# Performance work log

Hardware: AMD Instinct MI355X
Metric: run time of the kernel (lower is better)

## Reference

```python
import jax, jax.numpy as jnp
import numpy as np
from jax import lax

B = 512
P_KEEP = 0.5  # base dropout keep probability (p=0.5)


def conv(x, w, b, pad):
    y = lax.conv_general_dilated(x, w, (1, 1), [(pad, pad), (pad, pad)],
                                 dimension_numbers=('NCHW', 'OIHW', 'NCHW'))
    return y + b[None, :, None, None]


def maxpool3s2(x):
    return lax.reduce_window(x, -jnp.inf, lax.max, (1, 1, 3, 3), (1, 1, 2, 2), 'VALID')


def eb_linear(p_out, a, W):
    # Excitation backprop through a linear layer (bias ignored).
    # p_out: [B, out] marginal winning probs at layer output
    # a:     [B, in]  (non-negative) activations at layer input
    # W:     [out, in]
    Wp = jnp.maximum(W, 0.0)
    z = a @ Wp.T                              # [B, out]
    s = jnp.where(z > 0, p_out / z, 0.0)      # [B, out]
    return a * (s @ Wp)                       # [B, in]


def setup_inputs() -> dict:
    key = jax.random.key(0)
    ks = jax.random.split(key, 16)

    def w(k, shape, fan_in):
        return (jax.random.normal(k, shape, jnp.float32) / np.sqrt(fan_in)).astype(jnp.float32)

    return {
        'x': jax.random.normal(ks[0], (B, 3, 32, 32), jnp.float32),
        'noise': jax.random.uniform(ks[1], (B, 2048), jnp.float32),
        'conv1_w': w(ks[2], (96, 3, 5, 5), 3 * 25),
        'conv1_b': jnp.zeros((96,), jnp.float32),
        'conv2_w': w(ks[3], (128, 96, 5, 5), 96 * 25),
        'conv2_b': jnp.zeros((128,), jnp.float32),
        'conv3_w': w(ks[4], (256, 128, 5, 5), 128 * 25),
        'conv3_b': jnp.zeros((256,), jnp.float32),
        'fc1_w': w(ks[5], (2048, 1024), 1024),
        'fc1_b': jnp.zeros((2048,), jnp.float32),
        'fc2_w': w(ks[6], (2048, 2048), 2048),
        'fc2_b': jnp.zeros((2048,), jnp.float32),
        'fc3_w': w(ks[7], (10, 2048), 2048),
        'fc3_b': jnp.zeros((10,), jnp.float32),
        'label': jax.random.randint(ks[8], (B,), 0, 10),
    }


def reference(x, noise, conv1_w, conv1_b, conv2_w, conv2_b, conv3_w, conv3_b,
              fc1_w, fc1_b, fc2_w, fc2_b, fc3_w, fc3_b, label):
    h1 = maxpool3s2(jax.nn.relu(conv(x, conv1_w, conv1_b, 1)))   # [B,96,14,14]
    h2 = maxpool3s2(jax.nn.relu(conv(h1, conv2_w, conv2_b, 2)))  # [B,128,6,6]
    h3 = maxpool3s2(jax.nn.relu(conv(h2, conv3_w, conv3_b, 2)))  # [B,256,2,2]
    h4 = h3.reshape(h3.shape[0], -1)                             # [B,1024]
    h5 = jax.nn.relu(h4 @ fc1_w.T + fc1_b)                       # [B,2048]

    # --- Excitation backprop through latterModel (fc2 -> relu -> fc3), batched ---
    h6_eb = jax.nn.relu(h5 @ fc2_w.T + fc2_b)                    # [B,2048]
    p_out = jax.nn.one_hot(label, 10, dtype=h5.dtype)            # [B,10]
    p_h6 = eb_linear(p_out, h6_eb, fc3_w)                        # [B,2048]
    pebs = eb_linear(p_h6, h5, fc2_w)                            # [B,2048]

    # --- Excitation Dropout mask ---
    N = pebs.shape[1]
    num = (1.0 - P_KEEP) * (N - 1) * pebs
    retain_p = 1.0 - num / (num + P_KEEP * (1.0 - pebs))         # [B,2048]
    mask = (noise < retain_p).astype(h5.dtype)
    h_ed = jnp.where(retain_p > 0, h5 * mask / retain_p, 0.0)

    h6 = jax.nn.relu(h_ed @ fc2_w.T + fc2_b)                     # [B,2048]
    return h6 @ fc3_w.T + fc3_b                                  # [B,10]
```

## Files before the change

kernel.cpp:

```cpp
#include <hip/hip_runtime.h>
#include <hip/hip_bf16.h>


typedef __attribute__((ext_vector_type(8))) short bf16x8;
typedef __attribute__((ext_vector_type(4))) float f32x4;

__device__ __forceinline__ void split_bf16(float x, ushort& h, ushort& l) {
    __hip_bfloat16 bh = __float2bfloat16(x);
    float fh = __bfloat162float(bh);
    __hip_bfloat16 bl = __float2bfloat16(x - fh);
    h = *(ushort*)&bh;
    l = *(ushort*)&bl;
}

__device__ __forceinline__ void split3_bf16(float x, ushort& a, ushort& b,
                                            ushort& c) {
    __hip_bfloat16 ba = __float2bfloat16(x);
    float fa = __bfloat162float(ba);
    float r = x - fa;
    __hip_bfloat16 bb = __float2bfloat16(r);
    float fb = __bfloat162float(bb);
    __hip_bfloat16 bc = __float2bfloat16(r - fb);
    a = *(ushort*)&ba;
    b = *(ushort*)&bb;
    c = *(ushort*)&bc;
}

__device__ __forceinline__ void gld_lds16(const void* g, void* l) {
    __builtin_amdgcn_global_load_lds(
        (const __attribute__((address_space(1))) unsigned int*)g,
        (__attribute__((address_space(3))) unsigned int*)l, 16, 0, 0);
}

__global__ void zero_k(float4* __restrict__ p, int n4) {
    int idx = blockIdx.x * 256 + threadIdx.x;
    int stride = gridDim.x * 256;
    float4 z = {0.f, 0.f, 0.f, 0.f};
    for (int i = idx; i < n4; i += stride) p[i] = z;
}

__global__ void transw_k(const float* __restrict__ in, float* __restrict__ out,
                         int OC, int K) {
    int idx = blockIdx.x * 256 + threadIdx.x;
    if (idx >= OC * K) return;
    int oc = idx / K, k = idx % K;
    out[k * OC + oc] = in[idx];
}

__global__ void splitw_k(const float* __restrict__ in, ushort* __restrict__ hi,
                         ushort* __restrict__ lo, int OC, int IC) {
    int idx = blockIdx.x * 256 + threadIdx.x;
    if (idx >= OC * IC * 25) return;
    int oc = idx / (IC * 25);
    int r = idx % (IC * 25);
    int ic = r / 25, tap = r % 25;
    float v = in[idx];
    ushort h, l;
    split_bf16(v, h, l);
    size_t k = (size_t)oc * IC * 25 + tap * IC + ic;
    hi[k] = h;
    lo[k] = l;
}

__global__ void splitw3_k(const float* __restrict__ in, ushort* __restrict__ out,
                          int off, int total) {
    int idx = blockIdx.x * 256 + threadIdx.x;
    if (idx >= total) return;
    ushort a, b, c;
    split3_bf16(in[idx], a, b, c);
    out[idx] = a;
    out[idx + off] = b;
    out[idx + 2 * off] = c;
}

__global__ __launch_bounds__(256) void splitw3t_relu_k(
        const float* __restrict__ in, ushort* __restrict__ out, int off) {
    __shared__ float tile[64][65];
    const int bx = blockIdx.x & 31, by = blockIdx.x >> 5;
    const int j = threadIdx.x & 63, i0 = threadIdx.x >> 6;
    for (int i = i0; i < 64; i += 4)
        tile[i][j] = in[(size_t)(by * 64 + i) * 2048 + bx * 64 + j];
    __syncthreads();
    for (int r = i0; r < 64; r += 4) {
        float x = fmaxf(tile[j][r], 0.f);
        ushort a, b, c;
        split3_bf16(x, a, b, c);
        size_t o = (size_t)(bx * 64 + r) * 2048 + by * 64 + j;
        out[o] = a;
        out[o + off] = b;
        out[o + 2 * off] = c;
    }
}

__global__ __launch_bounds__(256) void conv1_v3(
        const float* __restrict__ x, const float* __restrict__ w1t,
        const float* __restrict__ b1, ushort* __restrict__ h1hi,
        ushort* __restrict__ h1lo) {
    __shared__ float simg[3 * 34 * 34];
    __shared__ float c1s[8][904];
    const int b = blockIdx.x, oc0 = blockIdx.y * 8, t = threadIdx.x;

    for (int i = t; i < 3 * 34 * 34; i += 256) simg[i] = 0.f;
    __syncthreads();
    for (int i = t; i < 3072; i += 256) {
        int ic = i >> 10, r = (i >> 5) & 31, c = i & 31;
        simg[ic * 1156 + (r + 1) * 34 + (c + 1)] = x[(size_t)b * 3072 + i];
    }
    __syncthreads();

    int base[4];
    bool valid[4];
#pragma unroll
    for (int j = 0; j < 4; j++) {
        int p = t + j * 256;
        valid[j] = p < 900;
        int oh = p / 30, ow = p % 30;
        base[j] = valid[j] ? oh * 34 + ow : 0;
    }

    float acc[4][8];
#pragma unroll
    for (int j = 0; j < 4; j++)
#pragma unroll
        for (int u = 0; u < 8; u++) acc[j][u] = 0.f;

#pragma unroll 1
    for (int ic = 0; ic < 3; ic++) {
        const int icb = ic * 1156;
#pragma unroll 1
        for (int kh = 0; kh < 5; kh++) {
#pragma unroll
            for (int kw = 0; kw < 5; kw++) {
                const float4* wr =
                    (const float4*)&w1t[(ic * 25 + kh * 5 + kw) * 96 + oc0];
                float4 w0 = wr[0], w1v = wr[1];
#pragma unroll
                for (int j = 0; j < 4; j++) {
                    float v = simg[icb + base[j] + kh * 34 + kw];
#pragma unroll
                    for (int u = 0; u < 4; u++) {
                        acc[j][u] = fmaf((&w0.x)[u], v, acc[j][u]);
                        acc[j][u + 4] = fmaf((&w1v.x)[u], v, acc[j][u + 4]);
                    }
                }
            }
        }
    }
#pragma unroll
    for (int j = 0; j < 4; j++)
        if (valid[j]) {
            int p = t + j * 256;
#pragma unroll
            for (int u = 0; u < 8; u++) c1s[u][p] = acc[j][u];
        }
    __syncthreads();
    if (t < 196) {
        const int ph = t / 14, pw = t % 14;
        ushort hv[8], lv[8];
#pragma unroll
        for (int u = 0; u < 8; u++) {
            float m = c1s[u][(2 * ph) * 30 + 2 * pw];
#pragma unroll
            for (int q = 1; q < 9; q++) {
                int dy = q / 3, dx = q % 3;
                m = fmaxf(m, c1s[u][(2 * ph + dy) * 30 + 2 * pw + dx]);
            }
            float o = fmaxf(m + b1[oc0 + u], 0.f);
            split_bf16(o, hv[u], lv[u]);
        }
        size_t ob = (((size_t)b * 18 + ph + 2) * 18 + pw + 2) * 96 + oc0;
        *(bf16x8*)&h1hi[ob] = *(bf16x8*)&hv[0];
        *(bf16x8*)&h1lo[ob] = *(bf16x8*)&lv[0];
    }
}

template <int BM, int IC, int H, int W, int OH, int OW, int OC, int NM>
__global__ __launch_bounds__(256, 2) void convmfma5_k(
        const ushort* __restrict__ ah, int aoff,
        const ushort* __restrict__ wh, int boff,
        const float* __restrict__ bias, float* __restrict__ C) {
    constexpr int K = 25 * IC;
    constexpr int MI = BM / 32;
    constexpr int G = NM * (OC / 128);
    __shared__ ushort At[2][BM * 64];
    __shared__ ushort Bt[2][128 * 64];
    const int t = threadIdx.x;
    const int lane = t & 63, wv = t >> 6;
    const int id = blockIdx.x;
    const int id2 = (id & 7) * (G >> 3) + (id >> 3);
    const int n0 = (id2 / NM) * 128;
    const int m0 = (id2 % NM) * BM;
    const int wm = (wv >> 1) * (BM / 2);
    const int wn = (wv & 1) * 64;

    const int srow = lane >> 3;
    const int slot = lane & 7;
    const int part = slot ^ srow;
    const bool hiA = part < 4;
    const int pk = (part & 3) * 8;

    int arb[MI];
#pragma unroll
    for (int rr = 0; rr < MI; rr++) {
        int r = wv * (BM / 4) + rr * 8 + srow;
        int m = m0 + r;
        int b = m / (OH * OW), pxy = m % (OH * OW);
        int oh = pxy / OW, ow = pxy % OW;
        arb[rr] = ((b * H + oh) * W + ow) * IC + pk;
    }
    const ushort* __restrict__ aptr = ah + (hiA ? 0 : aoff);
    size_t brb[4];
#pragma unroll
    for (int rr = 0; rr < 4; rr++) {
        int r = wv * 32 + rr * 8 + srow;
        brb[rr] = (size_t)(n0 + r) * K + pk;
    }
    const ushort* __restrict__ bptr = wh + (hiA ? 0 : boff);

    f32x4 acc[MI][4];
#pragma unroll
    for (int i = 0; i < MI; i++)
#pragma unroll
        for (int j = 0; j < 4; j++) acc[i][j] = (f32x4)(0.f);

    const int q = lane >> 4;
    const int fr = lane & 15;

    auto stage = [&](int buf, int k0s) {
        const int tap = k0s / IC;
        const int koff = ((tap / 5) * W + (tap % 5)) * IC + (k0s - tap * IC);
#pragma unroll
        for (int rr = 0; rr < MI; rr++)
            gld_lds16(aptr + arb[rr] + koff,
                      &At[buf][(wv * (BM / 4) + rr * 8) * 64]);
#pragma unroll
        for (int rr = 0; rr < 4; rr++)
            gld_lds16(bptr + brb[rr] + k0s,
                      &Bt[buf][(wv * 32 + rr * 8) * 64]);
    };

    stage(0, 0);
    __syncthreads();

    int cur = 0;
#pragma unroll 1
    for (int k0 = 0; k0 < K; k0 += 32) {
        bf16x8 afh[MI], afl[MI], bfh[4], bfl[4];
#pragma unroll
        for (int i = 0; i < MI; i++) {
            int row = wm + fr + i * 16;
            afh[i] = *(const bf16x8*)&At[cur][row * 64 + ((q ^ (row & 7)) << 3)];
            afl[i] = *(const bf16x8*)&At[cur][row * 64 + (((4 | q) ^ (row & 7)) << 3)];
        }
#pragma unroll
        for (int j = 0; j < 4; j++) {
            int row = wn + fr + j * 16;
            bfh[j] = *(const bf16x8*)&Bt[cur][row * 64 + ((q ^ (row & 7)) << 3)];
            bfl[j] = *(const bf16x8*)&Bt[cur][row * 64 + (((4 | q) ^ (row & 7)) << 3)];
        }
        const int nxt = k0 + 32;
        if (nxt < K) stage(cur ^ 1, nxt);

#pragma unroll
        for (int i = 0; i < MI; i++)
#pragma unroll
            for (int j = 0; j < 4; j++) {
                acc[i][j] = __builtin_amdgcn_mfma_f32_16x16x32_bf16(
                    afh[i], bfh[j], acc[i][j], 0, 0, 0);
                acc[i][j] = __builtin_amdgcn_mfma_f32_16x16x32_bf16(
                    afh[i], bfl[j], acc[i][j], 0, 0, 0);
                acc[i][j] = __builtin_amdgcn_mfma_f32_16x16x32_bf16(
                    afl[i], bfh[j], acc[i][j], 0, 0, 0);
            }
        __syncthreads();
        cur ^= 1;
    }

    const int crow0 = (lane >> 4) * 4;
    const int ccol = lane & 15;
#pragma unroll
    for (int i = 0; i < MI; i++) {
        int gm = m0 + wm + i * 16 + crow0;
#pragma unroll
        for (int j = 0; j < 4; j++) {
            int gn = n0 + wn + j * 16 + ccol;
            float bb = bias[gn];
#pragma unroll
            for (int r = 0; r < 4; r++)
                C[(size_t)(gm + r) * OC + gn] = acc[i][j][r] + bb;
        }
    }
}

__global__ void pool2_k(const float* __restrict__ in, ushort* __restrict__ ohi,
                        ushort* __restrict__ olo) {
    int idx = blockIdx.x * 256 + threadIdx.x;
    if (idx >= 512 * 36 * 128) return;
    int c = idx & 127;
    int tmp = idx >> 7;
    int pw = tmp % 6;
    int tmp2 = tmp / 6;
    int ph = tmp2 % 6;
    int b = tmp2 / 6;
    size_t base = (((size_t)b * 14 + 2 * ph) * 14 + 2 * pw) * 128 + c;
    float m = -3.4e38f;
#pragma unroll
    for (int dy = 0; dy < 3; dy++)
#pragma unroll
        for (int dx = 0; dx < 3; dx++)
            m = fmaxf(m, in[base + (dy * 14 + dx) * 128]);
    float v = fmaxf(m, 0.f);
    ushort h, l;
    split_bf16(v, h, l);
    size_t o = (((size_t)b * 10 + ph + 2) * 10 + pw + 2) * 128 + c;
    ohi[o] = h;
    olo[o] = l;
}

__global__ void pool3_k(const float* __restrict__ in, float* __restrict__ h3) {
    int idx = blockIdx.x * 256 + threadIdx.x;
    if (idx >= 512 * 4 * 256) return;
    int c = idx & 255;
    int pw = (idx >> 8) & 1;
    int ph = (idx >> 9) & 1;
    int b = idx >> 10;
    size_t base = (((size_t)b * 6 + 2 * ph) * 6 + 2 * pw) * 256 + c;
    float m = -3.4e38f;
#pragma unroll
    for (int dy = 0; dy < 3; dy++)
#pragma unroll
        for (int dx = 0; dx < 3; dx++)
            m = fmaxf(m, in[base + (dy * 6 + dx) * 256]);
    h3[(size_t)b * 1024 + c * 4 + ph * 2 + pw] = fmaxf(m, 0.f);
}

template <int BIAS, int RELUOUT, int DUAL>
__global__ __launch_bounds__(256, 2) void gemmfc_k(
        const float* __restrict__ A, const ushort* __restrict__ B3, int boff,
        const float* __restrict__ bias, float* __restrict__ C,
        float* __restrict__ C2, int K, int N) {
    __shared__ ushort Aa[32][44], Ab[32][44], Ac[32][44];
    __shared__ ushort Ba[64][44], Bb[64][44], Bc[64][44];
    const int t = threadIdx.x;
    const int n0 = blockIdx.x * 64;
    const int m0 = blockIdx.y * 32;
    const int lane = t & 63, wv = t >> 6;
    const int wm = (wv >> 1) * 16, wn = (wv & 1) * 32;
    const int fr = lane & 15, kp = (lane >> 4) * 8;

    f32x4 acc[2], acc2[DUAL ? 2 : 1];
#pragma unroll
    for (int j = 0; j < 2; j++) acc[j] = (f32x4)(0.f);
    if constexpr (DUAL) {
#pragma unroll
        for (int j = 0; j < 2; j++) acc2[j] = (f32x4)(0.f);
    }

    const int ar = t >> 2, ak = (t & 3) * 8;

    for (int k0 = 0; k0 < K; k0 += 32) {
        float4 a0, a1;
        if (t < 128) {
            a0 = *(const float4*)&A[(size_t)(m0 + ar) * K + k0 + ak];
            a1 = *(const float4*)&A[(size_t)(m0 + ar) * K + k0 + ak + 4];
        }
        size_t bidx = (size_t)(n0 + ar) * K + k0 + ak;
        bf16x8 b0 = *(const bf16x8*)&B3[bidx];
        bf16x8 b1 = *(const bf16x8*)&B3[bidx + boff];
        bf16x8 b2 = *(const bf16x8*)&B3[bidx + 2 * (size_t)boff];
        __syncthreads();
        if (t < 128) {
            ushort sa[8], sb[8], sc[8];
#pragma unroll
            for (int e = 0; e < 4; e++)
                split3_bf16((&a0.x)[e], sa[e], sb[e], sc[e]);
#pragma unroll
            for (int e = 0; e < 4; e++)
                split3_bf16((&a1.x)[e], sa[4 + e], sb[4 + e], sc[4 + e]);
            *(bf16x8*)&Aa[ar][ak] = *(bf16x8*)sa;
            *(bf16x8*)&Ab[ar][ak] = *(bf16x8*)sb;
            *(bf16x8*)&Ac[ar][ak] = *(bf16x8*)sc;
        }
        *(bf16x8*)&Ba[ar][ak] = b0;
        *(bf16x8*)&Bb[ar][ak] = b1;
        *(bf16x8*)&Bc[ar][ak] = b2;
        __syncthreads();

        bf16x8 fa = *(const bf16x8*)&Aa[wm + fr][kp];
        bf16x8 fb = *(const bf16x8*)&Ab[wm + fr][kp];
        bf16x8 fc = *(const bf16x8*)&Ac[wm + fr][kp];
#pragma unroll
        for (int j = 0; j < 2; j++) {
            int row = wn + j * 16 + fr;
            bf16x8 ga = *(const bf16x8*)&Ba[row][kp];
            bf16x8 gb = *(const bf16x8*)&Bb[row][kp];
            bf16x8 gc = *(const bf16x8*)&Bc[row][kp];
            acc[j] = __builtin_amdgcn_mfma_f32_16x16x32_bf16(fa, ga, acc[j], 0, 0, 0);
            acc[j] = __builtin_amdgcn_mfma_f32_16x16x32_bf16(fa, gb, acc[j], 0, 0, 0);
            acc[j] = __builtin_amdgcn_mfma_f32_16x16x32_bf16(fb, ga, acc[j], 0, 0, 0);
            acc[j] = __builtin_amdgcn_mfma_f32_16x16x32_bf16(fa, gc, acc[j], 0, 0, 0);
            acc[j] = __builtin_amdgcn_mfma_f32_16x16x32_bf16(fc, ga, acc[j], 0, 0, 0);
            acc[j] = __builtin_amdgcn_mfma_f32_16x16x32_bf16(fb, gb, acc[j], 0, 0, 0);
            if constexpr (DUAL) {
                bf16x8 msk = ga >> 15;
                bf16x8 ra = ga & ~msk;
                bf16x8 rb = gb & ~msk;
                bf16x8 rc = gc & ~msk;
                acc2[j] = __builtin_amdgcn_mfma_f32_16x16x32_bf16(fa, ra, acc2[j], 0, 0, 0);
                acc2[j] = __builtin_amdgcn_mfma_f32_16x16x32_bf16(fa, rb, acc2[j], 0, 0, 0);
                acc2[j] = __builtin_amdgcn_mfma_f32_16x16x32_bf16(fb, ra, acc2[j], 0, 0, 0);
                acc2[j] = __builtin_amdgcn_mfma_f32_16x16x32_bf16(fa, rc, acc2[j], 0, 0, 0);
                acc2[j] = __builtin_amdgcn_mfma_f32_16x16x32_bf16(fc, ra, acc2[j], 0, 0, 0);
                acc2[j] = __builtin_amdgcn_mfma_f32_16x16x32_bf16(fb, rb, acc2[j], 0, 0, 0);
            }
        }
    }

    const int gm0 = m0 + wm + (lane >> 4) * 4;
#pragma unroll
    for (int j = 0; j < 2; j++) {
        int gn = n0 + wn + j * 16 + fr;
        float bb = BIAS ? bias[gn] : 0.f;
#pragma unroll
        for (int r = 0; r < 4; r++) {
            float v = acc[j][r] + bb;
            if constexpr (RELUOUT) v = fmaxf(v, 0.f);
            C[(size_t)(gm0 + r) * N + gn] = v;
            if constexpr (DUAL) C2[(size_t)(gm0 + r) * N + gn] = acc2[j][r];
        }
    }
}

__global__ __launch_bounds__(256) void zlab_k(
        const float* __restrict__ h6eb, const float* __restrict__ w3,
        const int* __restrict__ label, float* __restrict__ zlab) {
    __shared__ float red[4];
    const int b = blockIdx.x, t = threadIdx.x;
    const int lab = label[b];
    const float4* hp = (const float4*)(h6eb + (size_t)b * 2048);
    const float4* wp = (const float4*)(w3 + (size_t)lab * 2048);
    float s = 0.f;
    for (int i = t; i < 512; i += 256) {
        float4 h = hp[i], w = wp[i];
        s += h.x * fmaxf(w.x, 0.f) + h.y * fmaxf(w.y, 0.f) +
             h.z * fmaxf(w.z, 0.f) + h.w * fmaxf(w.w, 0.f);
    }
#pragma unroll
    for (int off = 32; off > 0; off >>= 1) s += __shfl_down(s, off, 64);
    if ((t & 63) == 0) red[t >> 6] = s;
    __syncthreads();
    if (t == 0) zlab[b] = red[0] + red[1] + red[2] + red[3];
}

__global__ void s2_k(const float* __restrict__ h6eb, const float* __restrict__ z2,
                     const float* __restrict__ w3, const int* __restrict__ label,
                     const float* __restrict__ zlab, float* __restrict__ s2) {
    int idx = blockIdx.x * 256 + threadIdx.x;
    int b = idx >> 11, j = idx & 2047;
    float zl = zlab[b], zv = z2[idx];
    float v = 0.f;
    if (zl > 0.f && zv > 0.f) {
        float wp = fmaxf(w3[(size_t)label[b] * 2048 + j], 0.f);
        v = h6eb[idx] * wp / (zl * zv);
    }
    s2[idx] = v;
}

__global__ void edrop_k(const float* __restrict__ h5, const float* __restrict__ t,
                        const float* __restrict__ noise, float* __restrict__ hed) {
    int idx = blockIdx.x * 256 + threadIdx.x;
    float pe = h5[idx] * t[idx];
    float num = 1023.5f * pe;
    float retain = 1.f - num / (num + 0.5f * (1.f - pe));
    float m = (noise[idx] < retain) ? 1.f : 0.f;
    hed[idx] = (retain > 0.f) ? h5[idx] * m / retain : 0.f;
}

__global__ void fc3_out_k(const float* __restrict__ h6, const float* __restrict__ w,
                          const float* __restrict__ bias, float* __restrict__ out) {
    int idx = blockIdx.x * 256 + threadIdx.x;
    if (idx >= 5120) return;
    int b = idx / 10, c = idx % 10;
    const float4* hp = (const float4*)(h6 + (size_t)b * 2048);
    const float4* wp = (const float4*)(w + (size_t)c * 2048);
    float s = 0.f;
    for (int i = 0; i < 512; i++) {
        float4 h = hp[i], ww = wp[i];
        s += h.x * ww.x + h.y * ww.y + h.z * ww.z + h.w * ww.w;
    }
    out[idx] = s + bias[c];
}

extern "C" void kernel_launch(void* const* d_in, const int* in_sizes, int n_in,
                              void* d_out, int out_size, void* d_ws, size_t ws_size,
                              hipStream_t stream) {
    const float* x       = (const float*)d_in[0];
    const float* noise   = (const float*)d_in[1];
    const float* conv1_w = (const float*)d_in[2];
    const float* conv1_b = (const float*)d_in[3];
    const float* conv2_w = (const float*)d_in[4];
    const float* conv2_b = (const float*)d_in[5];
    const float* conv3_w = (const float*)d_in[6];
    const float* conv3_b = (const float*)d_in[7];
    const float* fc1_w   = (const float*)d_in[8];
    const float* fc1_b   = (const float*)d_in[9];
    const float* fc2_w   = (const float*)d_in[10];
    const float* fc2_b   = (const float*)d_in[11];
    const float* fc3_w   = (const float*)d_in[12];
    const float* fc3_b   = (const float*)d_in[13];
    const int*   label   = (const int*)d_in[14];
    float* out = (float*)d_out;

    const size_t N_H1 = (size_t)512 * 18 * 18 * 96;
    const size_t N_C2 = (size_t)512 * 14 * 14 * 128;
    const size_t N_H2 = (size_t)512 * 10 * 10 * 128;
    const size_t N_H3 = (size_t)512 * 1024;

    float* ws = (float*)d_ws;
    ushort* h1hi = (ushort*)ws;
    ushort* h1lo = h1hi + N_H1;
    float* c3 = ws;
    float* c2 = ws + N_H1;
    float* h5   = c2;
    float* h6eb = c2 + 1 * 1048576;
    float* z2   = c2 + 2 * 1048576;
    float* s2   = c2 + 3 * 1048576;
    float* tb   = c2 + 4 * 1048576;
    float* hed  = c2 + 5 * 1048576;
    float* h6   = c2 + 6 * 1048576;
    float* zlab = c2 + 7 * 1048576;
    ushort* h2hi = (ushort*)(ws + N_H1 + N_C2);
    ushort* h2lo = h2hi + N_H2;
    float* h3  = ws + N_H1 + N_C2 + N_H2;
    float* w1t = h3 + N_H3;
    ushort* w2sh = (ushort*)(w1t + 7200);
    ushort* w2sl = w2sh + 307200;
    ushort* w3sh = w2sl + 307200;
    ushort* w3sl = w3sh + 819200;
    ushort* w23  = w3sl + 819200;
    ushort* w2rt = w23 + 3 * 4194304;
    ushort* w13  = w2rt + 3 * 4194304;

    transw_k<<<(75 * 96 + 255) / 256, 256, 0, stream>>>(conv1_w, w1t, 96, 75);
    splitw_k<<<(307200 + 255) / 256, 256, 0, stream>>>(conv2_w, w2sh, w2sl, 128, 96);
    splitw_k<<<(819200 + 255) / 256, 256, 0, stream>>>(conv3_w, w3sh, w3sl, 256, 128);
    splitw3_k<<<16384, 256, 0, stream>>>(fc2_w, w23, 4194304, 4194304);
    splitw3t_relu_k<<<1024, 256, 0, stream>>>(fc2_w, w2rt, 4194304);
    splitw3_k<<<8192, 256, 0, stream>>>(fc1_w, w13, 2097152, 2097152);

    zero_k<<<2048, 256, 0, stream>>>((float4*)h1hi, (int)(N_H1 / 4));
    zero_k<<<2048, 256, 0, stream>>>((float4*)h2hi, (int)(N_H2 / 4));

    conv1_v3<<<dim3(512, 12), 256, 0, stream>>>(x, w1t, conv1_b, h1hi, h1lo);
    convmfma5_k<128, 96, 18, 18, 14, 14, 128, 784><<<784, 256, 0, stream>>>(
        h1hi, (int)N_H1, w2sh, 307200, conv2_b, c2);
    pool2_k<<<(512 * 36 * 128 + 255) / 256, 256, 0, stream>>>(c2, h2hi, h2lo);
    convmfma5_k<64, 128, 10, 10, 6, 6, 256, 288><<<576, 256, 0, stream>>>(
        h2hi, (int)N_H2, w3sh, 819200, conv3_b, c3);
    pool3_k<<<(512 * 4 * 256 + 255) / 256, 256, 0, stream>>>(c3, h3);

    gemmfc_k<1, 1, 0><<<dim3(32, 16), 256, 0, stream>>>(
        h3, w13, 2097152, fc1_b, h5, nullptr, 1024, 2048);

    gemmfc_k<1, 1, 1><<<dim3(32, 16), 256, 0, stream>>>(
        h5, w23, 4194304, fc2_b, h6eb, z2, 2048, 2048);

    zlab_k<<<512, 256, 0, stream>>>(h6eb, fc3_w, label, zlab);
    s2_k<<<4096, 256, 0, stream>>>(h6eb, z2, fc3_w, label, zlab, s2);

    gemmfc_k<0, 0, 0><<<dim3(32, 16), 256, 0, stream>>>(
        s2, w2rt, 4194304, nullptr, tb, nullptr, 2048, 2048);

    edrop_k<<<4096, 256, 0, stream>>>(h5, tb, noise, hed);

    gemmfc_k<1, 1, 0><<<dim3(32, 16), 256, 0, stream>>>(
        hed, w23, 4194304, fc2_b, h6, nullptr, 2048, 2048);

    fc3_out_k<<<20, 256, 0, stream>>>(h6, fc3_w, fc3_b, out);
}
```

Measured before the change: 821.6 us.

## Split conv MFMA kernels into 8-wave conv2 and single-buffered-B conv3 variants

The conv2 implicit-GEMM kernel now runs 512 threads (8 waves) per 128x128 tile, so each wave holds a 32x64 sub-tile with fewer accumulators and staging loads. The conv3 kernel keeps a 64x128 tile but single-buffers the weight tile in LDS, adding an extra barrier, and raises the launch bound to 3 blocks per CU. Both changes aim to raise occupancy and latency hiding. The cost is more barriers per K step in conv3 and the loss of some overlap on weight staging.

```diff
diff --git a/kernel.cpp b/kernel.cpp
--- a/kernel.cpp
+++ b/kernel.cpp
@@ -174,23 +174,22 @@
     }
 }
 
-template <int BM, int IC, int H, int W, int OH, int OW, int OC, int NM>
-__global__ __launch_bounds__(256, 2) void convmfma5_k(
+template <int IC, int H, int W, int OH, int OW, int OC, int NM>
+__global__ __launch_bounds__(512, 2) void convmfma8_k(
         const ushort* __restrict__ ah, int aoff,
         const ushort* __restrict__ wh, int boff,
         const float* __restrict__ bias, float* __restrict__ C) {
     constexpr int K = 25 * IC;
-    constexpr int MI = BM / 32;
     constexpr int G = NM * (OC / 128);
-    __shared__ ushort At[2][BM * 64];
+    __shared__ ushort At[2][128 * 64];
     __shared__ ushort Bt[2][128 * 64];
     const int t = threadIdx.x;
     const int lane = t & 63, wv = t >> 6;
     const int id = blockIdx.x;
     const int id2 = (id & 7) * (G >> 3) + (id >> 3);
     const int n0 = (id2 / NM) * 128;
-    const int m0 = (id2 % NM) * BM;
-    const int wm = (wv >> 1) * (BM / 2);
+    const int m0 = (id2 % NM) * 128;
+    const int wm = (wv >> 1) * 32;
     const int wn = (wv & 1) * 64;
 
     const int srow = lane >> 3;
@@ -199,27 +198,27 @@
     const bool hiA = part < 4;
     const int pk = (part & 3) * 8;
 
-    int arb[MI];
-#pragma unroll
-    for (int rr = 0; rr < MI; rr++) {
-        int r = wv * (BM / 4) + rr * 8 + srow;
+    int arb[2];
+#pragma unroll
+    for (int rr = 0; rr < 2; rr++) {
+        int r = wv * 16 + rr * 8 + srow;
         int m = m0 + r;
         int b = m / (OH * OW), pxy = m % (OH * OW);
         int oh = pxy / OW, ow = pxy % OW;
         arb[rr] = ((b * H + oh) * W + ow) * IC + pk;
     }
     const ushort* __restrict__ aptr = ah + (hiA ? 0 : aoff);
-    size_t brb[4];
-#pragma unroll
-    for (int rr = 0; rr < 4; rr++) {
-        int r = wv * 32 + rr * 8 + srow;
+    size_t brb[2];
+#pragma unroll
+    for (int rr = 0; rr < 2; rr++) {
+        int r = wv * 16 + rr * 8 + srow;
         brb[rr] = (size_t)(n0 + r) * K + pk;
     }
     const ushort* __restrict__ bptr = wh + (hiA ? 0 : boff);
 
-    f32x4 acc[MI][4];
-#pragma unroll
-    for (int i = 0; i < MI; i++)
+    f32x4 acc[2][4];
+#pragma unroll
+    for (int i = 0; i < 2; i++)
 #pragma unroll
         for (int j = 0; j < 4; j++) acc[i][j] = (f32x4)(0.f);
 
@@ -230,13 +229,11 @@
         const int tap = k0s / IC;
         const int koff = ((tap / 5) * W + (tap % 5)) * IC + (k0s - tap * IC);
 #pragma unroll
-        for (int rr = 0; rr < MI; rr++)
-            gld_lds16(aptr + arb[rr] + koff,
-                      &At[buf][(wv * (BM / 4) + rr * 8) * 64]);
-#pragma unroll
-        for (int rr = 0; rr < 4; rr++)
-            gld_lds16(bptr + brb[rr] + k0s,
-                      &Bt[buf][(wv * 32 + rr * 8) * 64]);
+        for (int rr = 0; rr < 2; rr++)
+            gld_lds16(aptr + arb[rr] + koff, &At[buf][(wv * 16 + rr * 8) * 64]);
+#pragma unroll
+        for (int rr = 0; rr < 2; rr++)
+            gld_lds16(bptr + brb[rr] + k0s, &Bt[buf][(wv * 16 + rr * 8) * 64]);
     };
 
     stage(0, 0);
@@ -245,9 +242,9 @@
     int cur = 0;
 #pragma unroll 1
     for (int k0 = 0; k0 < K; k0 += 32) {
-        bf16x8 afh[MI], afl[MI], bfh[4], bfl[4];
-#pragma unroll
-        for (int i = 0; i < MI; i++) {
+        bf16x8 afh[2], afl[2], bfh[4], bfl[4];
+#pragma unroll
+        for (int i = 0; i < 2; i++) {
             int row = wm + fr + i * 16;
             afh[i] = *(const bf16x8*)&At[cur][row * 64 + ((q ^ (row & 7)) << 3)];
             afl[i] = *(const bf16x8*)&At[cur][row * 64 + (((4 | q) ^ (row & 7)) << 3)];
@@ -262,7 +259,7 @@
         if (nxt < K) stage(cur ^ 1, nxt);
 
 #pragma unroll
-        for (int i = 0; i < MI; i++)
+        for (int i = 0; i < 2; i++)
 #pragma unroll
             for (int j = 0; j < 4; j++) {
                 acc[i][j] = __builtin_amdgcn_mfma_f32_16x16x32_bf16(
@@ -279,7 +276,129 @@
     const int crow0 = (lane >> 4) * 4;
     const int ccol = lane & 15;
 #pragma unroll
-    for (int i = 0; i < MI; i++) {
+    for (int i = 0; i < 2; i++) {
+        int gm = m0 + wm + i * 16 + crow0;
+#pragma unroll
+        for (int j = 0; j < 4; j++) {
+            int gn = n0 + wn + j * 16 + ccol;
+            float bb = bias[gn];
+#pragma unroll
+            for (int r = 0; r < 4; r++)
+                C[(size_t)(gm + r) * OC + gn] = acc[i][j][r] + bb;
+        }
+    }
+}
+
+template <int IC, int H, int W, int OH, int OW, int OC, int NM>
+__global__ __launch_bounds__(256, 3) void convmfma9_k(
+        const ushort* __restrict__ ah, int aoff,
+        const ushort* __restrict__ wh, int boff,
+        const float* __restrict__ bias, float* __restrict__ C) {
+    constexpr int K = 25 * IC;
+    constexpr int G = NM * (OC / 128);
+    __shared__ ushort At[2][64 * 64];
+    __shared__ ushort Bt[128 * 64];
+    const int t = threadIdx.x;
+    const int lane = t & 63, wv = t >> 6;
+    const int id = blockIdx.x;
+    const int id2 = (id & 7) * (G >> 3) + (id >> 3);
+    const int n0 = (id2 / NM) * 128;
+    const int m0 = (id2 % NM) * 64;
+    const int wm = (wv >> 1) * 32;
+    const int wn = (wv & 1) * 64;
+
+    const int srow = lane >> 3;
+    const int slot = lane & 7;
+    const int part = slot ^ srow;
+    const bool hiA = part < 4;
+    const int pk = (part & 3) * 8;
+
+    int arb[2];
+#pragma unroll
+    for (int rr = 0; rr < 2; rr++) {
+        int r = wv * 16 + rr * 8 + srow;
+        int m = m0 + r;
+        int b = m / (OH * OW), pxy = m % (OH * OW);
+        int oh = pxy / OW, ow = pxy % OW;
+        arb[rr] = ((b * H + oh) * W + ow) * IC + pk;
+    }
+    const ushort* __restrict__ aptr = ah + (hiA ? 0 : aoff);
+    size_t brb[4];
+#pragma unroll
+    for (int rr = 0; rr < 4; rr++) {
+        int r = wv * 32 + rr * 8 + srow;
+        brb[rr] = (size_t)(n0 + r) * K + pk;
+    }
+    const ushort* __restrict__ bptr = wh + (hiA ? 0 : boff);
+
+    f32x4 acc[2][4];
+#pragma unroll
+    for (int i = 0; i < 2; i++)
+#pragma unroll
+        for (int j = 0; j < 4; j++) acc[i][j] = (f32x4)(0.f);
+
+    const int q = lane >> 4;
+    const int fr = lane & 15;
+
+    auto stageA = [&](int buf, int k0s) {
+        const int tap = k0s / IC;
+        const int koff = ((tap / 5) * W + (tap % 5)) * IC + (k0s - tap * IC);
+#pragma unroll
+        for (int rr = 0; rr < 2; rr++)
+            gld_lds16(aptr + arb[rr] + koff, &At[buf][(wv * 16 + rr * 8) * 64]);
+    };
+    auto stageB = [&](int k0s) {
+#pragma unroll
+        for (int rr = 0; rr < 4; rr++)
+            gld_lds16(bptr + brb[rr] + k0s, &Bt[(wv * 32 + rr * 8) * 64]);
+    };
+
+    stageA(0, 0);
+    stageB(0);
+    __syncthreads();
+
+    int cur = 0;
+#pragma unroll 1
+    for (int k0 = 0; k0 < K; k0 += 32) {
+        bf16x8 bfh[4], bfl[4];
+#pragma unroll
+        for (int j = 0; j < 4; j++) {
+            int row = wn + fr + j * 16;
+            bfh[j] = *(const bf16x8*)&Bt[row * 64 + ((q ^ (row & 7)) << 3)];
+            bfl[j] = *(const bf16x8*)&Bt[row * 64 + (((4 | q) ^ (row & 7)) << 3)];
+        }
+        __syncthreads();
+        const int nxt = k0 + 32;
+        if (nxt < K) {
+            stageA(cur ^ 1, nxt);
+            stageB(nxt);
+        }
+        bf16x8 afh[2], afl[2];
+#pragma unroll
+        for (int i = 0; i < 2; i++) {
+            int row = wm + fr + i * 16;
+            afh[i] = *(const bf16x8*)&At[cur][row * 64 + ((q ^ (row & 7)) << 3)];
+            afl[i] = *(const bf16x8*)&At[cur][row * 64 + (((4 | q) ^ (row & 7)) << 3)];
+        }
+#pragma unroll
+        for (int i = 0; i < 2; i++)
+#pragma unroll
+            for (int j = 0; j < 4; j++) {
+                acc[i][j] = __builtin_amdgcn_mfma_f32_16x16x32_bf16(
+                    afh[i], bfh[j], acc[i][j], 0, 0, 0);
+                acc[i][j] = __builtin_amdgcn_mfma_f32_16x16x32_bf16(
+                    afh[i], bfl[j], acc[i][j], 0, 0, 0);
+                acc[i][j] = __builtin_amdgcn_mfma_f32_16x16x32_bf16(
+                    afl[i], bfh[j], acc[i][j], 0, 0, 0);
+            }
+        __syncthreads();
+        cur ^= 1;
+    }
+
+    const int crow0 = (lane >> 4) * 4;
+    const int ccol = lane & 15;
+#pragma unroll
+    for (int i = 0; i < 2; i++) {
         int gm = m0 + wm + i * 16 + crow0;
 #pragma unroll
         for (int j = 0; j < 4; j++) {
@@ -552,10 +671,10 @@
     zero_k<<<2048, 256, 0, stream>>>((float4*)h2hi, (int)(N_H2 / 4));
 
     conv1_v3<<<dim3(512, 12), 256, 0, stream>>>(x, w1t, conv1_b, h1hi, h1lo);
-    convmfma5_k<128, 96, 18, 18, 14, 14, 128, 784><<<784, 256, 0, stream>>>(
+    convmfma8_k<96, 18, 18, 14, 14, 128, 784><<<784, 512, 0, stream>>>(
         h1hi, (int)N_H1, w2sh, 307200, conv2_b, c2);
     pool2_k<<<(512 * 36 * 128 + 255) / 256, 256, 0, stream>>>(c2, h2hi, h2lo);
-    convmfma5_k<64, 128, 10, 10, 6, 6, 256, 288><<<576, 256, 0, stream>>>(
+    convmfma9_k<128, 10, 10, 6, 6, 256, 288><<<576, 256, 0, stream>>>(
         h2hi, (int)N_H2, w3sh, 819200, conv3_b, c3);
     pool3_k<<<(512 * 4 * 256 + 255) / 256, 256, 0, stream>>>(c3, h3);
 
```

Result: no change. 811.1 us (-1.3%).
